# Performance work log

Measured on AMD Instinct MI355X. Metric: run time of the kernel, lower is better.

Reference implementation:

```python
import jax, jax.numpy as jnp
from jax import lax
import numpy as np

NSTEP, NGRID, MU = 365, 4000, 8
STAIND = NSTEP - 1          # time index providing static parameters
TDLST = [1, 2, 3, 4, 5]     # 1-based indices of dynamic parameters
HBV_LO = jnp.array([0.0, 1.0, 0.005, 0.005, 0.0, 0.0, 0.005, 0.005, 0.0, 0.0, 0.0], jnp.float32)
HBV_HI = jnp.array([1.0, 2000.0, 0.995, 0.995, 1.0, 7.0, 0.995, 0.995, 1.0, 1.0, 1.0], jnp.float32)
SMIN = 1e-4                 # clamp floor for states
CAPMIN = 0.005 / 4          # floor for derived capacities

# ---- MARRMoT-style flux helpers (all elementwise) ----

def split_1(p1, In):
    return p1 * In

def soilmoisture_1(S1, S1max, S2, S2max):
    mask = (S1 / S1max < S2 / S2max).astype(S1.dtype)
    return (S2 * S1max - S1 * S2max) / (S1max + S2max) * mask

def soilmoisture_2(S1, S1max, S2, S2max, S3, S3max):
    # water rebalance to equal relative storage (3 stores); flux drawn from S2
    mask = (S1 / S1max < (S2 + S3) / (S2max + S3max)).astype(S1.dtype)
    return (S2 * S1max - S1 * S2max) / (S1max + S2max + S3max) * mask

def evap_7(S, Smax, Ep, dt):
    return jnp.minimum(S / Smax * Ep, S / dt)

def evap_1(S, Ep, dt):
    return jnp.minimum(Ep, S / dt)

def saturation_1(In, S, Smax):
    return In * (S >= Smax).astype(In.dtype)

def interflow_5(p1, S):
    return p1 * S

def baseflow_1(p1, S):
    return p1 * S

def percolation_4(pbase, zperc, rexp, deficit, defmax, S, Smax, dt):
    pc = pbase * (1.0 + zperc * (deficit / defmax) ** (1.0 + rexp)) * S / Smax
    return jnp.maximum(0.0, jnp.minimum(pc, S / dt))

def deficit_dist(S1, S1max, S2, S2max):
    d1 = jnp.maximum(0.0, 1.0 - S1 / S1max)
    d2 = jnp.maximum(0.0, 1.0 - S2 / S2max)
    tot = d1 + d2
    return jnp.where(tot > 0, d1 / jnp.where(tot > 0, tot, 1.0), S1max / (S1max + S2max))


def _forward(x, parameters):
    Nstep, Ngrid = x.shape[0], x.shape[1]
    mu = parameters.shape[3]
    P_ = x[:, :, 0]   # [Nstep, Ngrid]
    Ep_ = x[:, :, 2]  # [Nstep, Ngrid]

    # scale raw [0,1] params to physical ranges
    parT = HBV_LO[None, None, :, None] + parameters * (HBV_HI - HBV_LO)[None, None, :, None]
    parsta = parT[STAIND]  # [Ngrid, 11, mu] static params
    dyn = np.zeros(11, dtype=bool)
    for ix in TDLST:
        dyn[ix - 1] = True
    dyn = jnp.asarray(dyn)
    # dydrop=0 -> dynamic params always used on tdlst slots, static elsewhere
    parhbv = jnp.where(dyn[None, None, :, None], parT, parsta[None])  # [Nstep,Ngrid,11,mu]

    S0 = jnp.full((Ngrid, mu), 0.001, x.dtype)

    def step(carry, inp):
        S1, S2, S3, S4, S5 = carry
        Pt, Ept, par = inp            # par: [Ngrid, 11, mu]
        P = Pt[:, None]               # [Ngrid, 1] broadcasts against [Ngrid, mu]
        Ep = Ept[:, None]
        pctim, smax, f1, f2, kuz, rexp, f3, f4, pfree, klzp, klzs = [par[:, i, :] for i in range(11)]

        uztwm = f1 * smax
        uzfwm = jnp.maximum(CAPMIN, f2 * (smax - uztwm))
        lztwm = jnp.maximum(CAPMIN, f3 * (smax - uztwm - uzfwm))
        lzfwpm = jnp.maximum(CAPMIN, f4 * (smax - uztwm - uzfwm - lztwm))
        lzfwsm = jnp.maximum(CAPMIN, (1.0 - f4) * (smax - uztwm - uzfwm - lztwm))
        pbase = lzfwpm * klzp + lzfwsm * klzs
        denom = lzfwsm * klzs + lzfwpm * klzp
        zperc = jnp.minimum(1e5, (lztwm + lzfwsm * (1.0 - klzs)) / denom + lzfwpm * (1.0 - klzp) / denom)
        dt = 1.0

        flux_qdir = split_1(pctim, P)
        flux_peff = split_1(1.0 - pctim, P)
        flux_ru = soilmoisture_1(S1, uztwm, S2, uzfwm)
        flux_euztw = evap_7(S1, uztwm, Ep, dt)
        flux_twexu = saturation_1(flux_peff, S1, uztwm)
        flux_qsur = saturation_1(flux_twexu, S2, uzfwm)
        flux_qint = interflow_5(kuz, S2)
        flux_euzfw = evap_1(S2, jnp.maximum(0.0, Ep - flux_euztw), dt)
        deficit = (jnp.maximum(1e-8, lztwm - S3) + jnp.maximum(1e-8, lzfwpm - S4)
                   + jnp.maximum(1e-8, lzfwsm - S5))
        defmax = jnp.maximum(1e-8, lztwm + lzfwpm + lzfwsm)
        flux_pc = percolation_4(pbase, zperc, rexp, deficit, defmax, S2, uzfwm, dt)
        flux_pctw = split_1(1.0 - pfree, flux_pc)
        flux_elztw = evap_7(S3, lztwm, jnp.maximum(0.0, Ep - flux_euztw - flux_euzfw), dt)
        flux_twexl = saturation_1(flux_pctw, S3, lztwm)
        fp = deficit_dist(S4, lzfwpm, S5, lzfwsm)
        fs = deficit_dist(S5, lzfwsm, S4, lzfwpm)
        flux_twexlp = split_1(fp, flux_twexl)
        flux_twexls = split_1(fs, flux_twexl)
        flux_pcfwp = split_1(pfree * fp, flux_pc)
        flux_pcfws = split_1(pfree * fs, flux_pc)
        flux_rlp = soilmoisture_2(S3, lztwm, S4, lzfwpm, S5, lzfwsm)
        flux_rls = soilmoisture_2(S3, lztwm, S5, lzfwsm, S4, lzfwpm)
        flux_qbfp = baseflow_1(klzp, S4)
        flux_qbfs = baseflow_1(klzs, S5)

        nS1 = jnp.maximum(S1 + flux_peff + flux_ru - flux_euztw - flux_twexu, SMIN)
        nS2 = jnp.maximum(S2 + flux_twexu - flux_euzfw - flux_qsur - flux_qint - flux_ru - flux_pc, SMIN)
        nS3 = jnp.maximum(S3 + flux_pctw + flux_rlp + flux_rls - flux_elztw - flux_twexl, SMIN)
        nS4 = jnp.maximum(S4 + flux_twexlp + flux_pcfwp - flux_rlp - flux_qbfp, SMIN)
        nS5 = jnp.maximum(S5 + flux_twexls + flux_pcfws - flux_rls - flux_qbfs, SMIN)

        qsim = flux_qdir + flux_qsur + flux_qint + flux_qbfp + flux_qbfs
        et = flux_euztw + flux_euzfw + flux_elztw
        return (nS1, nS2, nS3, nS4, nS5), (qsim, et)

    _, (Qsimmu, ETmu) = lax.scan(step, (S0, S0, S0, S0, S0), (P_, Ep_, parhbv))
    Qs = Qsimmu.mean(-1, keepdims=True)      # muwts=None -> mean over components
    ETave = ETmu.mean(-1, keepdims=True)
    return jnp.concatenate([Qs, ETave], axis=-1)  # [Nstep, Ngrid, 2]


def setup_inputs() -> dict:
    key = jax.random.key(0)
    k1, k2 = jax.random.split(key)
    x = jax.random.uniform(k1, (NSTEP, NGRID, 3), dtype=jnp.float32)
    parameters = jax.random.uniform(k2, (NSTEP, NGRID, 11, MU), dtype=jnp.float32)
    return {"x": x, "parameters": parameters}


def reference(x, parameters):
    return _forward(x, parameters)
```

## Files before the change

kernel.cpp:

```cpp
#include <hip/hip_runtime.h>
#include <stdint.h>

#define NSTEP 365
#define NGRID 4000
#define CAPMIN 0.00125f
#define SMINV 0.0001f

#define BUF_DW 384
#define NSLOT 20
#define PSTR_DW (NGRID * 88)
#define XSTR_DW (NGRID * 3)

typedef __attribute__((address_space(3))) uint32_t lds_u32_t;
typedef __attribute__((address_space(1))) uint32_t glb_u32_t;

__device__ __forceinline__ void dma4(const float* g, float* l) {
    __builtin_amdgcn_global_load_lds((const glb_u32_t*)(const void*)g,
                                     (lds_u32_t*)(void*)l, 4, 0, 0);
}

__device__ __forceinline__ float frcp(float x) { return __builtin_amdgcn_rcpf(x); }
__device__ __forceinline__ float fexp2(float x) { return __builtin_amdgcn_exp2f(x); }
__device__ __forceinline__ float flog2(float x) { return __builtin_amdgcn_logf(x); }

__device__ __forceinline__ void sac_step(
    float c0, float c1, float c2, float c3, float c4,
    float P, float Ep,
    float e1, float f3, float f4, float pfree, float klzp, float klzs,
    float& S1, float& S2, float& S3, float& S4, float& S5,
    float& qsim, float& et)
{
    const float pctim = c0;
    const float smax  = 1.0f + c1 * 1999.0f;
    const float f1    = 0.005f + c2 * 0.99f;
    const float f2    = 0.005f + c3 * 0.99f;
    const float kuz   = c4;

    const float uztwm = f1 * smax;
    float rem = smax - uztwm;
    const float uzfwm = fmaxf(CAPMIN, f2 * rem);
    rem = rem - uzfwm;
    const float lztwm = fmaxf(CAPMIN, f3 * rem);
    rem = rem - lztwm;
    const float lzfwpm = fmaxf(CAPMIN, f4 * rem);
    const float lzfwsm = fmaxf(CAPMIN, (1.0f - f4) * rem);
    const float pbase  = lzfwpm * klzp + lzfwsm * klzs;
    const float invden = frcp(pbase);
    const float zperc  = fminf(100000.0f,
        (lztwm + lzfwsm * (1.0f - klzs) + lzfwpm * (1.0f - klzp)) * invden);

    const float inv_uztwm = frcp(uztwm);
    const float inv_uzfwm = frcp(uzfwm);
    const float inv_lztwm = frcp(lztwm);

    const float qdir = pctim * P;
    const float peff = (1.0f - pctim) * P;

    const float ru = (S1 * inv_uztwm < S2 * inv_uzfwm)
        ? (S2 * uztwm - S1 * uzfwm) * frcp(uztwm + uzfwm) : 0.0f;

    const float euztw = fminf(S1 * inv_uztwm * Ep, S1);
    const float twexu = (S1 >= uztwm) ? peff : 0.0f;
    const float qsur  = (S2 >= uzfwm) ? twexu : 0.0f;
    const float qint  = kuz * S2;
    const float euzfw = fminf(fmaxf(0.0f, Ep - euztw), S2);

    const float deficit = fmaxf(1e-8f, lztwm - S3)
                        + fmaxf(1e-8f, lzfwpm - S4)
                        + fmaxf(1e-8f, lzfwsm - S5);
    const float defmax     = lztwm + lzfwpm + lzfwsm;
    const float inv_defmax = frcp(defmax);
    const float ratio      = deficit * inv_defmax;
    const float powterm    = fexp2(e1 * flog2(ratio));
    float pc = pbase * (1.0f + zperc * powterm) * S2 * inv_uzfwm;
    pc = fmaxf(0.0f, fminf(pc, S2));

    const float pctw  = (1.0f - pfree) * pc;
    const float elztw = fminf(S3 * inv_lztwm * fmaxf(0.0f, Ep - euztw - euzfw), S3);
    const float twexl = (S3 >= lztwm) ? pctw : 0.0f;

    const float d1  = fmaxf(0.0f, 1.0f - S4 * frcp(lzfwpm));
    const float d2  = fmaxf(0.0f, 1.0f - S5 * frcp(lzfwsm));
    const float tot = d1 + d2;
    const float pm  = lzfwpm + lzfwsm;
    const float num = (tot > 0.0f) ? d1 : lzfwpm;
    const float den = (tot > 0.0f) ? tot : pm;
    const float fp  = num * frcp(den);
    const float fs  = 1.0f - fp;

    const float twexlp = fp * twexl;
    const float twexls = fs * twexl;
    const float pcfwp  = pfree * fp * pc;
    const float pcfws  = pfree * fs * pc;

    const float invpm = frcp(pm);
    const float s3r   = S3 * inv_lztwm;
    const bool rlmask = s3r < (S4 + S5) * invpm;
    const float rlp = rlmask ? (S4 * lztwm - S3 * lzfwpm) * inv_defmax : 0.0f;
    const float rls = rlmask ? (S5 * lztwm - S3 * lzfwsm) * inv_defmax : 0.0f;

    const float qbfp = klzp * S4;
    const float qbfs = klzs * S5;

    S1 = fmaxf(S1 + peff + ru - euztw - twexu, SMINV);
    S2 = fmaxf(S2 + twexu - euzfw - qsur - qint - ru - pc, SMINV);
    S3 = fmaxf(S3 + pctw + rlp + rls - elztw - twexl, SMINV);
    S4 = fmaxf(S4 + twexlp + pcfwp - rlp - qbfp, SMINV);
    S5 = fmaxf(S5 + twexls + pcfws - rls - qbfs, SMINV);

    qsim = qdir + qsur + qint + qbfp + qbfs;
    et   = euztw + euzfw + elztw;
}

__device__ __forceinline__ void issue_slot(const float* pp, const float* px,
                                           int t, float* dst) {
    const float* pj = pp + (size_t)t * PSTR_DW;
    dma4(pj,      dst);
    dma4(pj + 8,  dst + 64);
    dma4(pj + 16, dst + 128);
    dma4(pj + 24, dst + 192);
    dma4(pj + 32, dst + 256);
    dma4(px + (size_t)t * XSTR_DW, dst + 320);
}

__global__ __launch_bounds__(128, 1) void sacsma_kernel(
    const float* __restrict__ x,
    const float* __restrict__ par,
    float* __restrict__ out)
{
    __shared__ __align__(16) float lds[NSLOT * BUF_DW];
    __shared__ __align__(16) float smq[5 * 64];
    __shared__ __align__(16) float sme[5 * 64];

    const int wave = threadIdx.x >> 6;
    const int lane = threadIdx.x & 63;
    const int g0   = blockIdx.x * 8;

    if (wave == 0) {
        const int gl = lane >> 3;
        const int mu = lane & 7;
        const float* pp = par + (size_t)(g0 + gl) * 88 + mu;
        int xl = lane; if (xl >= 24) xl -= 24; if (xl >= 24) xl -= 24;
        const int xq = xl / 3;
        const float* px = x + (g0 + xq) * 3 + (xl - xq * 3);

        #pragma unroll
        for (int j = 0; j < 10; ++j)
            issue_slot(pp, px, j, lds + j * BUF_DW);

        for (int i = 0; i < NSTEP / 5; ++i) {
            asm volatile("s_waitcnt vmcnt(30)" ::: "memory");
            float* dst = lds + (((i + 2) & 3) * 5) * BUF_DW;
            int tb = 5 * (i + 2);
            if (tb >= NSTEP) tb -= NSTEP;
            #pragma unroll
            for (int j = 0; j < 5; ++j)
                issue_slot(pp, px, tb + j, dst + j * BUF_DW);
            __builtin_amdgcn_s_barrier();
        }
    } else {
        const int gl = lane >> 3;
        const int mu = lane & 7;
        const int g  = g0 + gl;

        const float* ps = par + ((size_t)(NSTEP - 1) * NGRID + g) * 88 + mu;
        const float e1    = 1.0f + ps[5 * 8] * 7.0f;
        const float f3    = 0.005f + ps[6 * 8] * 0.99f;
        const float f4    = 0.005f + ps[7 * 8] * 0.99f;
        const float pfree = ps[8 * 8];
        const float klzp  = ps[9 * 8];
        const float klzs  = ps[10 * 8];

        float S1 = 0.001f, S2 = 0.001f, S3 = 0.001f, S4 = 0.001f, S5 = 0.001f;

        for (int i = 0; i < NSTEP / 5; ++i) {
            __builtin_amdgcn_s_barrier();
            const int rbase = (i & 3) * (5 * BUF_DW);
            const int tbase = i * 5;

            #pragma unroll
            for (int j = 0; j < 5; ++j) {
                const float* sb = lds + rbase + j * BUF_DW;
                const float c0 = sb[lane];
                const float c1 = sb[64 + lane];
                const float c2 = sb[128 + lane];
                const float c3 = sb[192 + lane];
                const float c4 = sb[256 + lane];
                const float P  = sb[320 + gl * 3];
                const float Ep = sb[322 + gl * 3];
                float qs, ev;
                sac_step(c0, c1, c2, c3, c4, P, Ep,
                         e1, f3, f4, pfree, klzp, klzs,
                         S1, S2, S3, S4, S5, qs, ev);
                smq[j * 64 + lane] = qs;
                sme[j * 64 + lane] = ev;
            }

            if (lane < 40) {
                const int s  = lane >> 3;
                const int gg = lane & 7;
                const float4* q4 = reinterpret_cast<const float4*>(&smq[s * 64 + gg * 8]);
                const float4* e4 = reinterpret_cast<const float4*>(&sme[s * 64 + gg * 8]);
                const float4 qa = q4[0], qb = q4[1];
                const float4 ea = e4[0], eb = e4[1];
                const float qsum = ((qa.x + qa.y) + (qa.z + qa.w))
                                 + ((qb.x + qb.y) + (qb.z + qb.w));
                const float esum = ((ea.x + ea.y) + (ea.z + ea.w))
                                 + ((eb.x + eb.y) + (eb.z + eb.w));
                float2 o = make_float2(qsum * 0.125f, esum * 0.125f);
                *reinterpret_cast<float2*>(
                    out + ((size_t)(tbase + s) * NGRID + g0 + gg) * 2) = o;
            }
        }
    }
}

extern "C" void kernel_launch(void* const* d_in, const int* in_sizes, int n_in,
                              void* d_out, int out_size, void* d_ws, size_t ws_size,
                              hipStream_t stream) {
    const float* x   = (const float*)d_in[0];
    const float* par = (const float*)d_in[1];
    float* out = (float*)d_out;

    sacsma_kernel<<<NGRID / 8, 128, 0, stream>>>(x, par, out);
}
```

Measured before the change: 129.6 us.

## Split state-independent parameter derivation into a separate producer wave pipeline

Adds a third wave that computes the per-step derived capacities, reciprocals and fluxes that do not depend on state. It takes raw DMA'd data from LDS and writes packed derived values back to LDS. The recurrence wave then runs only the state-dependent chain, with some algebraic simplification: the zperc division is folded into pbase, the deficit fractions are cross-multiplied, and the rl mask comparison no longer uses reciprocals. This shortens the serial critical path per step. The cost is a three-stage barrier pipeline with more LDS traffic and a shallower DMA prefetch, since the loader now waits on vmcnt(0) each iteration.

After: 121.6 us. 1.07x faster.

```diff
diff --git a/kernel.cpp b/kernel.cpp
--- a/kernel.cpp
+++ b/kernel.cpp
@@ -5,11 +5,16 @@
 #define NGRID 4000
 #define CAPMIN 0.00125f
 #define SMINV 0.0001f
-
-#define BUF_DW 384
-#define NSLOT 20
 #define PSTR_DW (NGRID * 88)
 #define XSTR_DW (NGRID * 3)
+
+#define RAW_SLOT 384
+#define RAW_REG  (5 * RAW_SLOT)
+#define DER_SLOT 960
+#define DER_REG  (5 * DER_SLOT)
+#define DER_BASE 5760
+#define SMQ_BASE 15360
+#define SME_BASE 15680
 
 typedef __attribute__((address_space(3))) uint32_t lds_u32_t;
 typedef __attribute__((address_space(1))) uint32_t glb_u32_t;
@@ -22,95 +27,6 @@
 __device__ __forceinline__ float frcp(float x) { return __builtin_amdgcn_rcpf(x); }
 __device__ __forceinline__ float fexp2(float x) { return __builtin_amdgcn_exp2f(x); }
 __device__ __forceinline__ float flog2(float x) { return __builtin_amdgcn_logf(x); }
-
-__device__ __forceinline__ void sac_step(
-    float c0, float c1, float c2, float c3, float c4,
-    float P, float Ep,
-    float e1, float f3, float f4, float pfree, float klzp, float klzs,
-    float& S1, float& S2, float& S3, float& S4, float& S5,
-    float& qsim, float& et)
-{
-    const float pctim = c0;
-    const float smax  = 1.0f + c1 * 1999.0f;
-    const float f1    = 0.005f + c2 * 0.99f;
-    const float f2    = 0.005f + c3 * 0.99f;
-    const float kuz   = c4;
-
-    const float uztwm = f1 * smax;
-    float rem = smax - uztwm;
-    const float uzfwm = fmaxf(CAPMIN, f2 * rem);
-    rem = rem - uzfwm;
-    const float lztwm = fmaxf(CAPMIN, f3 * rem);
-    rem = rem - lztwm;
-    const float lzfwpm = fmaxf(CAPMIN, f4 * rem);
-    const float lzfwsm = fmaxf(CAPMIN, (1.0f - f4) * rem);
-    const float pbase  = lzfwpm * klzp + lzfwsm * klzs;
-    const float invden = frcp(pbase);
-    const float zperc  = fminf(100000.0f,
-        (lztwm + lzfwsm * (1.0f - klzs) + lzfwpm * (1.0f - klzp)) * invden);
-
-    const float inv_uztwm = frcp(uztwm);
-    const float inv_uzfwm = frcp(uzfwm);
-    const float inv_lztwm = frcp(lztwm);
-
-    const float qdir = pctim * P;
-    const float peff = (1.0f - pctim) * P;
-
-    const float ru = (S1 * inv_uztwm < S2 * inv_uzfwm)
-        ? (S2 * uztwm - S1 * uzfwm) * frcp(uztwm + uzfwm) : 0.0f;
-
-    const float euztw = fminf(S1 * inv_uztwm * Ep, S1);
-    const float twexu = (S1 >= uztwm) ? peff : 0.0f;
-    const float qsur  = (S2 >= uzfwm) ? twexu : 0.0f;
-    const float qint  = kuz * S2;
-    const float euzfw = fminf(fmaxf(0.0f, Ep - euztw), S2);
-
-    const float deficit = fmaxf(1e-8f, lztwm - S3)
-                        + fmaxf(1e-8f, lzfwpm - S4)
-                        + fmaxf(1e-8f, lzfwsm - S5);
-    const float defmax     = lztwm + lzfwpm + lzfwsm;
-    const float inv_defmax = frcp(defmax);
-    const float ratio      = deficit * inv_defmax;
-    const float powterm    = fexp2(e1 * flog2(ratio));
-    float pc = pbase * (1.0f + zperc * powterm) * S2 * inv_uzfwm;
-    pc = fmaxf(0.0f, fminf(pc, S2));
-
-    const float pctw  = (1.0f - pfree) * pc;
-    const float elztw = fminf(S3 * inv_lztwm * fmaxf(0.0f, Ep - euztw - euzfw), S3);
-    const float twexl = (S3 >= lztwm) ? pctw : 0.0f;
-
-    const float d1  = fmaxf(0.0f, 1.0f - S4 * frcp(lzfwpm));
-    const float d2  = fmaxf(0.0f, 1.0f - S5 * frcp(lzfwsm));
-    const float tot = d1 + d2;
-    const float pm  = lzfwpm + lzfwsm;
-    const float num = (tot > 0.0f) ? d1 : lzfwpm;
-    const float den = (tot > 0.0f) ? tot : pm;
-    const float fp  = num * frcp(den);
-    const float fs  = 1.0f - fp;
-
-    const float twexlp = fp * twexl;
-    const float twexls = fs * twexl;
-    const float pcfwp  = pfree * fp * pc;
-    const float pcfws  = pfree * fs * pc;
-
-    const float invpm = frcp(pm);
-    const float s3r   = S3 * inv_lztwm;
-    const bool rlmask = s3r < (S4 + S5) * invpm;
-    const float rlp = rlmask ? (S4 * lztwm - S3 * lzfwpm) * inv_defmax : 0.0f;
-    const float rls = rlmask ? (S5 * lztwm - S3 * lzfwsm) * inv_defmax : 0.0f;
-
-    const float qbfp = klzp * S4;
-    const float qbfs = klzs * S5;
-
-    S1 = fmaxf(S1 + peff + ru - euztw - twexu, SMINV);
-    S2 = fmaxf(S2 + twexu - euzfw - qsur - qint - ru - pc, SMINV);
-    S3 = fmaxf(S3 + pctw + rlp + rls - elztw - twexl, SMINV);
-    S4 = fmaxf(S4 + twexlp + pcfwp - rlp - qbfp, SMINV);
-    S5 = fmaxf(S5 + twexls + pcfws - rls - qbfs, SMINV);
-
-    qsim = qdir + qsur + qint + qbfp + qbfs;
-    et   = euztw + euzfw + elztw;
-}
 
 __device__ __forceinline__ void issue_slot(const float* pp, const float* px,
                                            int t, float* dst) {
@@ -123,94 +39,207 @@
     dma4(px + (size_t)t * XSTR_DW, dst + 320);
 }
 
-__global__ __launch_bounds__(128, 1) void sacsma_kernel(
+__global__ __launch_bounds__(192, 1) void sacsma_kernel(
     const float* __restrict__ x,
     const float* __restrict__ par,
     float* __restrict__ out)
 {
-    __shared__ __align__(16) float lds[NSLOT * BUF_DW];
-    __shared__ __align__(16) float smq[5 * 64];
-    __shared__ __align__(16) float sme[5 * 64];
+    __shared__ __align__(16) float lds[16000];
 
     const int wave = threadIdx.x >> 6;
     const int lane = threadIdx.x & 63;
     const int g0   = blockIdx.x * 8;
+    const int gl   = lane >> 3;
+    const int mu   = lane & 7;
+    const int g    = g0 + gl;
 
     if (wave == 0) {
-        const int gl = lane >> 3;
-        const int mu = lane & 7;
-        const float* pp = par + (size_t)(g0 + gl) * 88 + mu;
+        const float* pp = par + (size_t)g * 88 + mu;
         int xl = lane; if (xl >= 24) xl -= 24; if (xl >= 24) xl -= 24;
         const int xq = xl / 3;
         const float* px = x + (g0 + xq) * 3 + (xl - xq * 3);
 
         #pragma unroll
-        for (int j = 0; j < 10; ++j)
-            issue_slot(pp, px, j, lds + j * BUF_DW);
-
-        for (int i = 0; i < NSTEP / 5; ++i) {
-            asm volatile("s_waitcnt vmcnt(30)" ::: "memory");
-            float* dst = lds + (((i + 2) & 3) * 5) * BUF_DW;
-            int tb = 5 * (i + 2);
-            if (tb >= NSTEP) tb -= NSTEP;
-            #pragma unroll
-            for (int j = 0; j < 5; ++j)
-                issue_slot(pp, px, tb + j, dst + j * BUF_DW);
-            __builtin_amdgcn_s_barrier();
+        for (int j = 0; j < 5; ++j)
+            issue_slot(pp, px, j, lds + j * RAW_SLOT);
+
+        for (int i = 0; i < 75; ++i) {
+            asm volatile("s_waitcnt vmcnt(0)" ::: "memory");
+            if (i <= 71) {
+                const int b = i + 1;
+                float* dst = lds + (b % 3) * RAW_REG;
+                const int tb = 5 * b;
+                #pragma unroll
+                for (int j = 0; j < 5; ++j)
+                    issue_slot(pp, px, tb + j, dst + j * RAW_SLOT);
+            }
+            asm volatile("s_barrier" ::: "memory");
+        }
+    } else if (wave == 1) {
+        const float* ps = par + ((size_t)(NSTEP - 1) * NGRID + g) * 88 + mu;
+        const float f3   = 0.005f + ps[6 * 8] * 0.99f;
+        const float f4   = 0.005f + ps[7 * 8] * 0.99f;
+        const float klzp = ps[9 * 8];
+        const float klzs = ps[10 * 8];
+
+        for (int i = 0; i < 75; ++i) {
+            if (i >= 1 && i <= 73) {
+                const int b = i - 1;
+                const float* rreg = lds + (b % 3) * RAW_REG;
+                float* dreg = lds + DER_BASE + (b & 1) * DER_REG;
+                #pragma unroll
+                for (int j = 0; j < 5; ++j) {
+                    const float* rb = rreg + j * RAW_SLOT;
+                    float* db = dreg + j * DER_SLOT;
+
+                    const float c0 = rb[lane];
+                    const float c1 = rb[64 + lane];
+                    const float c2 = rb[128 + lane];
+                    const float c3 = rb[192 + lane];
+                    const float c4 = rb[256 + lane];
+                    const float P  = rb[320 + gl * 3];
+                    const float Ep = rb[322 + gl * 3];
+
+                    const float smaxv = 1.0f + c1 * 1999.0f;
+                    const float f1 = 0.005f + c2 * 0.99f;
+                    const float f2 = 0.005f + c3 * 0.99f;
+                    const float uztwm = f1 * smaxv;
+                    float rem = smaxv - uztwm;
+                    const float uzfwm = fmaxf(CAPMIN, f2 * rem);
+                    rem -= uzfwm;
+                    const float lztwm = fmaxf(CAPMIN, f3 * rem);
+                    rem -= lztwm;
+                    const float lzfwpm = fmaxf(CAPMIN, f4 * rem);
+                    const float lzfwsm = fmaxf(CAPMIN, (1.0f - f4) * rem);
+                    const float pbase = lzfwpm * klzp + lzfwsm * klzs;
+                    const float pz = fminf(lztwm + lzfwsm * (1.0f - klzs)
+                                           + lzfwpm * (1.0f - klzp),
+                                           100000.0f * pbase);
+                    const float inv_uztwm = frcp(uztwm);
+                    const float inv_uzfwm = frcp(uzfwm);
+                    const float inv_lztwm = frcp(lztwm);
+                    const float inv_uzsum = frcp(uztwm + uzfwm);
+                    const float qdir = c0 * P;
+                    const float peff = (1.0f - c0) * P;
+
+                    float2* d2 = reinterpret_cast<float2*>(db);
+                    d2[0 * 64 + lane] = make_float2(qdir, peff);
+                    d2[1 * 64 + lane] = make_float2(Ep, c4);
+                    d2[2 * 64 + lane] = make_float2(uztwm, uzfwm);
+                    d2[3 * 64 + lane] = make_float2(inv_uztwm, inv_uzfwm);
+                    d2[4 * 64 + lane] = make_float2(inv_uzsum, lztwm);
+                    d2[5 * 64 + lane] = make_float2(inv_lztwm, pbase);
+                    d2[6 * 64 + lane] = make_float2(lzfwpm, lzfwsm);
+                    db[896 + lane] = pz;
+                }
+                asm volatile("s_waitcnt lgkmcnt(0)" ::: "memory");
+            }
+            asm volatile("s_barrier" ::: "memory");
         }
     } else {
-        const int gl = lane >> 3;
-        const int mu = lane & 7;
-        const int g  = g0 + gl;
-
         const float* ps = par + ((size_t)(NSTEP - 1) * NGRID + g) * 88 + mu;
         const float e1    = 1.0f + ps[5 * 8] * 7.0f;
-        const float f3    = 0.005f + ps[6 * 8] * 0.99f;
-        const float f4    = 0.005f + ps[7 * 8] * 0.99f;
         const float pfree = ps[8 * 8];
         const float klzp  = ps[9 * 8];
         const float klzs  = ps[10 * 8];
 
         float S1 = 0.001f, S2 = 0.001f, S3 = 0.001f, S4 = 0.001f, S5 = 0.001f;
-
-        for (int i = 0; i < NSTEP / 5; ++i) {
-            __builtin_amdgcn_s_barrier();
-            const int rbase = (i & 3) * (5 * BUF_DW);
-            const int tbase = i * 5;
-
-            #pragma unroll
-            for (int j = 0; j < 5; ++j) {
-                const float* sb = lds + rbase + j * BUF_DW;
-                const float c0 = sb[lane];
-                const float c1 = sb[64 + lane];
-                const float c2 = sb[128 + lane];
-                const float c3 = sb[192 + lane];
-                const float c4 = sb[256 + lane];
-                const float P  = sb[320 + gl * 3];
-                const float Ep = sb[322 + gl * 3];
-                float qs, ev;
-                sac_step(c0, c1, c2, c3, c4, P, Ep,
-                         e1, f3, f4, pfree, klzp, klzs,
-                         S1, S2, S3, S4, S5, qs, ev);
-                smq[j * 64 + lane] = qs;
-                sme[j * 64 + lane] = ev;
+        float* smq = lds + SMQ_BASE;
+        float* sme = lds + SME_BASE;
+
+        for (int i = 0; i < 75; ++i) {
+            if (i >= 2) {
+                const int b = i - 2;
+                const float* dreg = lds + DER_BASE + (b & 1) * DER_REG;
+                #pragma unroll
+                for (int j = 0; j < 5; ++j) {
+                    const float* db = dreg + j * DER_SLOT;
+                    const float2* d2 = reinterpret_cast<const float2*>(db);
+                    const float2 v0 = d2[0 * 64 + lane];
+                    const float2 v1 = d2[1 * 64 + lane];
+                    const float2 v2 = d2[2 * 64 + lane];
+                    const float2 v3 = d2[3 * 64 + lane];
+                    const float2 v4 = d2[4 * 64 + lane];
+                    const float2 v5 = d2[5 * 64 + lane];
+                    const float2 v6 = d2[6 * 64 + lane];
+                    const float pz = db[896 + lane];
+                    const float qdir = v0.x, peff = v0.y;
+                    const float Ep = v1.x, kuz = v1.y;
+                    const float uztwm = v2.x, uzfwm = v2.y;
+                    const float inv_uztwm = v3.x, inv_uzfwm = v3.y;
+                    const float inv_uzsum = v4.x, lztwm = v4.y;
+                    const float inv_lztwm = v5.x, pbase = v5.y;
+                    const float lzfwpm = v6.x, lzfwsm = v6.y;
+
+                    const float rud = S2 * uztwm - S1 * uzfwm;
+                    const float ru  = (rud > 0.0f) ? rud * inv_uzsum : 0.0f;
+                    const float euztw = fminf(S1 * inv_uztwm * Ep, S1);
+                    const float twexu = (S1 >= uztwm) ? peff : 0.0f;
+                    const float qsur  = (S2 >= uzfwm) ? twexu : 0.0f;
+                    const float qint  = kuz * S2;
+                    const float euzfw = fminf(fmaxf(0.0f, Ep - euztw), S2);
+
+                    const float deficit = fmaxf(1e-8f, lztwm - S3)
+                                        + fmaxf(1e-8f, lzfwpm - S4)
+                                        + fmaxf(1e-8f, lzfwsm - S5);
+                    const float defmax = lztwm + lzfwpm + lzfwsm;
+                    const float inv_defmax = frcp(defmax);
+                    const float powterm = fexp2(e1 * flog2(deficit * inv_defmax));
+                    float pc = (pbase + pz * powterm) * S2 * inv_uzfwm;
+                    pc = fmaxf(0.0f, fminf(pc, S2));
+
+                    const float pctw  = (1.0f - pfree) * pc;
+                    const float elztw = fminf(S3 * inv_lztwm
+                                              * fmaxf(0.0f, Ep - euztw - euzfw), S3);
+                    const float twexl = (S3 >= lztwm) ? pctw : 0.0f;
+
+                    const float aa  = fmaxf(0.0f, lzfwpm - S4) * lzfwsm;
+                    const float bb  = fmaxf(0.0f, lzfwsm - S5) * lzfwpm;
+                    const float den = aa + bb;
+                    const float pm  = lzfwpm + lzfwsm;
+                    const float fp  = ((den > 0.0f) ? aa : lzfwpm)
+                                    * frcp((den > 0.0f) ? den : pm);
+                    const float fs  = 1.0f - fp;
+
+                    const float twexlp = fp * twexl;
+                    const float twexls = fs * twexl;
+                    const float pcfwp  = pfree * fp * pc;
+                    const float pcfws  = pfree * fs * pc;
+
+                    const bool rlm = S3 * pm < (S4 + S5) * lztwm;
+                    const float rlp = rlm ? (S4 * lztwm - S3 * lzfwpm) * inv_defmax : 0.0f;
+                    const float rls = rlm ? (S5 * lztwm - S3 * lzfwsm) * inv_defmax : 0.0f;
+
+                    const float qbfp = klzp * S4;
+                    const float qbfs = klzs * S5;
+
+                    S1 = fmaxf(S1 + peff + ru - euztw - twexu, SMINV);
+                    S2 = fmaxf(S2 + twexu - euzfw - qsur - qint - ru - pc, SMINV);
+                    S3 = fmaxf(S3 + pctw + rlp + rls - elztw - twexl, SMINV);
+                    S4 = fmaxf(S4 + twexlp + pcfwp - rlp - qbfp, SMINV);
+                    S5 = fmaxf(S5 + twexls + pcfws - rls - qbfs, SMINV);
+
+                    smq[j * 64 + lane] = qdir + qsur + qint + qbfp + qbfs;
+                    sme[j * 64 + lane] = euztw + euzfw + elztw;
+                }
+
+                if (lane < 40) {
+                    const int s  = lane >> 3;
+                    const int gg = lane & 7;
+                    const float4* q4 = reinterpret_cast<const float4*>(&smq[s * 64 + gg * 8]);
+                    const float4* e4 = reinterpret_cast<const float4*>(&sme[s * 64 + gg * 8]);
+                    const float4 qa = q4[0], qb = q4[1];
+                    const float4 ea = e4[0], eb = e4[1];
+                    const float qsum = ((qa.x + qa.y) + (qa.z + qa.w))
+                                     + ((qb.x + qb.y) + (qb.z + qb.w));
+                    const float esum = ((ea.x + ea.y) + (ea.z + ea.w))
+                                     + ((eb.x + eb.y) + (eb.z + eb.w));
+                    float2 o = make_float2(qsum * 0.125f, esum * 0.125f);
+                    *reinterpret_cast<float2*>(
+                        out + ((size_t)(5 * b + s) * NGRID + g0 + gg) * 2) = o;
+                }
             }
-
-            if (lane < 40) {
-                const int s  = lane >> 3;
-                const int gg = lane & 7;
-                const float4* q4 = reinterpret_cast<const float4*>(&smq[s * 64 + gg * 8]);
-                const float4* e4 = reinterpret_cast<const float4*>(&sme[s * 64 + gg * 8]);
-                const float4 qa = q4[0], qb = q4[1];
-                const float4 ea = e4[0], eb = e4[1];
-                const float qsum = ((qa.x + qa.y) + (qa.z + qa.w))
-                                 + ((qb.x + qb.y) + (qb.z + qb.w));
-                const float esum = ((ea.x + ea.y) + (ea.z + ea.w))
-                                 + ((eb.x + eb.y) + (eb.z + eb.w));
-                float2 o = make_float2(qsum * 0.125f, esum * 0.125f);
-                *reinterpret_cast<float2*>(
-                    out + ((size_t)(tbase + s) * NGRID + g0 + gg) * 2) = o;
-            }
+            asm volatile("s_barrier" ::: "memory");
         }
     }
 }
@@ -222,5 +251,5 @@
     const float* par = (const float*)d_in[1];
     float* out = (float*)d_out;
 
-    sacsma_kernel<<<NGRID / 8, 128, 0, stream>>>(x, par, out);
-}
+    sacsma_kernel<<<NGRID / 8, 192, 0, stream>>>(x, par, out);
+}
```
